# Kernel optimization log

Measured on AMD Instinct MI355X. Metric: run time of the kernel, lower is better.

## Reference

```python
import jax, jax.numpy as jnp
import numpy as np

AH, AW = 7, 7          # aligned_height, aligned_width
SCALE = 0.0625         # spatial_scale = 1/16
B, C, H, W, K = 2, 512, 64, 64, 2000


def setup_inputs() -> dict:
    key = jax.random.key(0)
    k1, k2, k3, k4 = jax.random.split(key, 4)
    features = jax.random.normal(k1, (B, C, H, W), dtype=jnp.float32)
    img = H / SCALE  # image-space extent = 1024
    bidx = jax.random.randint(k2, (K,), 0, B).astype(jnp.float32)
    xy1 = jax.random.uniform(k3, (K, 2), minval=0.0, maxval=img * 0.7)
    wh = jax.random.uniform(k4, (K, 2), minval=img * 0.05, maxval=img * 0.3)
    xy2 = jnp.minimum(xy1 + wh, img - 1.0)
    rois = jnp.concatenate(
        [bidx[:, None], xy1[:, 0:1], xy1[:, 1:2], xy2[:, 0:1], xy2[:, 1:2]], axis=1
    )
    return {"features": features, "rois": rois}


def _roi_align(features, rois, ph, pw, scale):
    # one bilinear sample per output pixel on a ph x pw grid, with
    # bin_size = roi_size / (p - 1), zero for out-of-bounds sample points.
    _, _, Hf, Wf = features.shape
    b = rois[:, 0].astype(jnp.int32)
    x1 = rois[:, 1] * scale
    y1 = rois[:, 2] * scale
    x2 = rois[:, 3] * scale
    y2 = rois[:, 4] * scale
    roi_w = jnp.maximum(x2 - x1, 0.0)
    roi_h = jnp.maximum(y2 - y1, 0.0)
    bin_h = roi_h / (ph - 1.0)
    bin_w = roi_w / (pw - 1.0)
    h = y1[:, None] + jnp.arange(ph, dtype=jnp.float32) * bin_h[:, None]  # [K,ph]
    w = x1[:, None] + jnp.arange(pw, dtype=jnp.float32) * bin_w[:, None]  # [K,pw]
    hs = jnp.minimum(jnp.floor(h), Hf - 2.0)
    ws = jnp.minimum(jnp.floor(w), Wf - 2.0)
    hr = h - hs  # interpolation ratios (match CUDA kernel exactly)
    wr = w - ws
    hi = jnp.clip(hs, 0, Hf - 2).astype(jnp.int32)
    wi = jnp.clip(ws, 0, Wf - 2).astype(jnp.int32)
    bK = b[:, None, None]          # [K,1,1]
    hK = hi[:, :, None]            # [K,ph,1]
    wK = wi[:, None, :]            # [K,1,pw]
    # advanced indexing: corner gathers -> [K,ph,pw,C]
    v00 = features[bK, :, hK, wK]
    v01 = features[bK, :, hK, wK + 1]
    v10 = features[bK, :, hK + 1, wK]
    v11 = features[bK, :, hK + 1, wK + 1]
    hrE = hr[:, :, None, None]
    wrE = wr[:, None, :, None]
    val = (v00 * (1 - hrE) * (1 - wrE)
           + v01 * (1 - hrE) * wrE
           + v10 * hrE * (1 - wrE)
           + v11 * hrE * wrE)
    valid = ((h >= 0) & (h < Hf))[:, :, None] & ((w >= 0) & (w < Wf))[:, None, :]
    val = jnp.where(valid[..., None], val, 0.0)
    return jnp.transpose(val, (0, 3, 1, 2))  # [K,C,ph,pw]


def reference(features, rois):
    # sample on (AH+1)x(AW+1) grid, then avg_pool2d(kernel=2, stride=1)
    x = _roi_align(features, rois, AH + 1, AW + 1, SCALE)  # [K,C,8,8]
    out = (x[:, :, :-1, :-1] + x[:, :, :-1, 1:]
           + x[:, :, 1:, :-1] + x[:, :, 1:, 1:]) * 0.25    # [K,C,7,7]
    return out
```

## Files before the change

kernel.cpp:

```cpp
#include <hip/hip_runtime.h>

#define HF 64
#define WF 64
#define CCH 512

typedef float f32x4 __attribute__((ext_vector_type(4)));

__device__ __forceinline__ unsigned short f32_to_bf16(float f) {
    unsigned int x = __float_as_uint(f);
    unsigned int r = (x + 0x7FFFu + ((x >> 16) & 1u)) >> 16;
    return (unsigned short)r;
}
__device__ __forceinline__ float bf16_to_f32(unsigned short u) {
    return __uint_as_float(((unsigned int)u) << 16);
}

__global__ __launch_bounds__(256) void nchw_to_nhwc_bf16(const float* __restrict__ src,
                                                         unsigned short* __restrict__ dst) {
    __shared__ float tile[32][33];
    const int hw0 = blockIdx.x * 32;
    const int c0  = blockIdx.y * 32;
    const int b   = blockIdx.z;
    const int tx  = threadIdx.x & 31;
    const int ty  = threadIdx.x >> 5;
    const float*    s = src + (size_t)b * CCH * (HF * WF);
    unsigned short* d = dst + (size_t)b * (HF * WF) * CCH;
#pragma unroll
    for (int i = 0; i < 32; i += 8)
        tile[ty + i][tx] = s[(size_t)(c0 + ty + i) * (HF * WF) + hw0 + tx];
    __syncthreads();
#pragma unroll
    for (int i = 0; i < 32; i += 8)
        d[(size_t)(hw0 + ty + i) * CCH + c0 + tx] = f32_to_bf16(tile[tx][ty + i]);
}

__global__ __launch_bounds__(256) void roialign_bf16(const unsigned short* __restrict__ ft,
                                                     const float* __restrict__ rois,
                                                     float* __restrict__ out) {
    __shared__ __align__(16) float sbuf[256 * 49];

    const int blk   = blockIdx.x;
    const int k     = blk >> 1;
    const int chunk = blk & 1;
    const int tid   = threadIdx.x;
    const int c     = chunk * 256 + tid;

    const float* r = rois + (size_t)k * 5;
    const int   b  = (int)r[0];
    const float x1 = r[1] * 0.0625f;
    const float y1 = r[2] * 0.0625f;
    const float x2 = r[3] * 0.0625f;
    const float y2 = r[4] * 0.0625f;
    const float bin_h = fmaxf(y2 - y1, 0.0f) / 7.0f;
    const float bin_w = fmaxf(x2 - x1, 0.0f) / 7.0f;

    int   hi_[8]; float hr_[8]; float fvh[8];
    int   wi_[8]; float wr_[8]; float fvw[8];
    unsigned colc[8];
#pragma unroll
    for (int i = 0; i < 8; ++i) {
        float h  = y1 + (float)i * bin_h;
        float hs = fminf(floorf(h), 62.0f);
        hr_[i]   = h - hs;
        hi_[i]   = (int)fminf(fmaxf(hs, 0.0f), 62.0f);
        fvh[i]   = (h >= 0.0f && h < 64.0f) ? 1.0f : 0.0f;
        float w  = x1 + (float)i * bin_w;
        float ws = fminf(floorf(w), 62.0f);
        wr_[i]   = w - ws;
        wi_[i]   = (int)fminf(fmaxf(ws, 0.0f), 62.0f);
        fvw[i]   = (w >= 0.0f && w < 64.0f) ? 1.0f : 0.0f;
        colc[i]  = (unsigned)(wi_[i] * CCH + c);
    }
    const unsigned bBase = (unsigned)(b * HF * WF * CCH);

    float TL[8], TR[8], BL[8], BR[8];
    int curR = -1000;

    float  prev[8];
    float* srow = sbuf + tid * 49;

#pragma unroll
    for (int i = 0; i < 8; ++i) {
        const int rr = hi_[i];
        if (rr == curR) {
        } else if (rr == curR + 1) {
#pragma unroll
            for (int j = 0; j < 8; ++j) { TL[j] = BL[j]; TR[j] = BR[j]; }
            const unsigned rb = bBase + (unsigned)((rr + 1) * WF * CCH);
#pragma unroll
            for (int j = 0; j < 8; ++j) {
                BL[j] = bf16_to_f32(ft[rb + colc[j]]);
                BR[j] = bf16_to_f32(ft[rb + colc[j] + CCH]);
            }
        } else {
            const unsigned rt = bBase + (unsigned)(rr * WF * CCH);
            const unsigned rb = rt + (unsigned)(WF * CCH);
#pragma unroll
            for (int j = 0; j < 8; ++j) {
                TL[j] = bf16_to_f32(ft[rt + colc[j]]);
                TR[j] = bf16_to_f32(ft[rt + colc[j] + CCH]);
            }
#pragma unroll
            for (int j = 0; j < 8; ++j) {
                BL[j] = bf16_to_f32(ft[rb + colc[j]]);
                BR[j] = bf16_to_f32(ft[rb + colc[j] + CCH]);
            }
        }
        curR = rr;

        float cur[8];
#pragma unroll
        for (int j = 0; j < 8; ++j) {
            const float top = TL[j] + wr_[j] * (TR[j] - TL[j]);
            const float bot = BL[j] + wr_[j] * (BR[j] - BL[j]);
            const float v   = top + hr_[i] * (bot - top);
            cur[j] = v * (fvh[i] * fvw[j]);
        }
        if (i > 0) {
#pragma unroll
            for (int j = 0; j < 7; ++j)
                srow[(i - 1) * 7 + j] =
                    0.25f * (prev[j] + prev[j + 1] + cur[j] + cur[j + 1]);
        }
#pragma unroll
        for (int j = 0; j < 8; ++j) prev[j] = cur[j];
    }

    __builtin_amdgcn_wave_barrier();

    const int wid  = tid >> 6;
    const int lane = tid & 63;
    float* obase = out + ((size_t)k * CCH + (size_t)chunk * 256 + (size_t)wid * 64) * 49;
    const f32x4* s4 = reinterpret_cast<const f32x4*>(sbuf + (size_t)wid * 64 * 49);
    f32x4*       o4 = reinterpret_cast<f32x4*>(obase);
    for (int idx = lane; idx < 784; idx += 64)
        __builtin_nontemporal_store(s4[idx], &o4[idx]);
}

__global__ __launch_bounds__(256) void roialign_f32_nchw(const float* __restrict__ ft,
                                                         const float* __restrict__ rois,
                                                         float* __restrict__ out) {
    __shared__ __align__(16) float sbuf[256 * 49];
    const int blk   = blockIdx.x;
    const int k     = blk >> 1;
    const int chunk = blk & 1;
    const int tid   = threadIdx.x;
    const int c     = chunk * 256 + tid;

    const float* r = rois + (size_t)k * 5;
    const int   b  = (int)r[0];
    const float x1 = r[1] * 0.0625f;
    const float y1 = r[2] * 0.0625f;
    const float x2 = r[3] * 0.0625f;
    const float y2 = r[4] * 0.0625f;
    const float bin_h = fmaxf(y2 - y1, 0.0f) / 7.0f;
    const float bin_w = fmaxf(x2 - x1, 0.0f) / 7.0f;

    int hi_[8]; float hr_[8]; float fvh[8];
    int wi_[8]; float wr_[8]; float fvw[8];
#pragma unroll
    for (int i = 0; i < 8; ++i) {
        float h  = y1 + (float)i * bin_h;
        float hs = fminf(floorf(h), 62.0f);
        hr_[i] = h - hs;
        hi_[i] = (int)fminf(fmaxf(hs, 0.0f), 62.0f);
        fvh[i] = (h >= 0.0f && h < 64.0f) ? 1.0f : 0.0f;
        float w  = x1 + (float)i * bin_w;
        float ws = fminf(floorf(w), 62.0f);
        wr_[i] = w - ws;
        wi_[i] = (int)fminf(fmaxf(ws, 0.0f), 62.0f);
        fvw[i] = (w >= 0.0f && w < 64.0f) ? 1.0f : 0.0f;
    }

    float prev[8];
    float* srow = sbuf + tid * 49;
#pragma unroll
    for (int i = 0; i < 8; ++i) {
        float cur[8];
#pragma unroll
        for (int j = 0; j < 8; ++j) {
            size_t o00 = (size_t)(b * CCH + c) * (HF * WF) + hi_[i] * WF + wi_[j];
            const float v00 = ft[o00];
            const float v01 = ft[o00 + 1];
            const float v10 = ft[o00 + WF];
            const float v11 = ft[o00 + WF + 1];
            const float top = v00 + wr_[j] * (v01 - v00);
            const float bot = v10 + wr_[j] * (v11 - v10);
            const float v   = top + hr_[i] * (bot - top);
            cur[j] = v * (fvh[i] * fvw[j]);
        }
        if (i > 0) {
#pragma unroll
            for (int j = 0; j < 7; ++j)
                srow[(i - 1) * 7 + j] =
                    0.25f * (prev[j] + prev[j + 1] + cur[j] + cur[j + 1]);
        }
#pragma unroll
        for (int j = 0; j < 8; ++j) prev[j] = cur[j];
    }
    __syncthreads();
    float* obase = out + ((size_t)k * CCH + (size_t)chunk * 256) * 49;
    const f32x4* s4 = reinterpret_cast<const f32x4*>(sbuf);
    f32x4*       o4 = reinterpret_cast<f32x4*>(obase);
    for (int idx = tid; idx < 3136; idx += 256) o4[idx] = s4[idx];
}

extern "C" void kernel_launch(void* const* d_in, const int* in_sizes, int n_in,
                              void* d_out, int out_size, void* d_ws, size_t ws_size,
                              hipStream_t stream) {
    const float* feat = (const float*)d_in[0];
    const float* rois = (const float*)d_in[1];
    float*       out  = (float*)d_out;

    const int B = in_sizes[0] / (CCH * HF * WF);
    const int K = in_sizes[1] / 5;

    const size_t tbytes = (size_t)B * CCH * HF * WF * sizeof(unsigned short);
    if (ws_size >= tbytes) {
        unsigned short* ftr = (unsigned short*)d_ws;
        dim3 tg((HF * WF) / 32, CCH / 32, B);
        nchw_to_nhwc_bf16<<<tg, 256, 0, stream>>>(feat, ftr);
        roialign_bf16<<<K * 2, 256, 0, stream>>>(ftr, rois, out);
    } else {
        roialign_f32_nchw<<<K * 2, 256, 0, stream>>>(feat, rois, out);
    }
}
```

Before: 66.43 us.

## Prefetch next ROI row corners and scalarize uniform row indices

The bf16 ROI-align kernel now loads the next bottom-row corners one iteration ahead, so the gathers overlap with the current row's interpolation. Row indices, ratios and column offsets are forced into scalar registers with readfirstlane, and launch bounds request 3 waves per SIMD. This targets gather latency and VGPR pressure, at the cost of extra registers for the prefetch buffers and possible spilling under the tighter launch bound.

New measurement: 71.49 us. +7.6%, slower.

```diff
diff --git a/kernel.cpp b/kernel.cpp
--- a/kernel.cpp
+++ b/kernel.cpp
@@ -13,6 +13,10 @@
 }
 __device__ __forceinline__ float bf16_to_f32(unsigned short u) {
     return __uint_as_float(((unsigned int)u) << 16);
+}
+__device__ __forceinline__ int   rfl_i(int x)   { return __builtin_amdgcn_readfirstlane(x); }
+__device__ __forceinline__ float rfl_f(float x) {
+    return __int_as_float(__builtin_amdgcn_readfirstlane(__float_as_int(x)));
 }
 
 __global__ __launch_bounds__(256) void nchw_to_nhwc_bf16(const float* __restrict__ src,
@@ -34,9 +38,9 @@
         d[(size_t)(hw0 + ty + i) * CCH + c0 + tx] = f32_to_bf16(tile[tx][ty + i]);
 }
 
-__global__ __launch_bounds__(256) void roialign_bf16(const unsigned short* __restrict__ ft,
-                                                     const float* __restrict__ rois,
-                                                     float* __restrict__ out) {
+__global__ __launch_bounds__(256, 3) void roialign_bf16(const unsigned short* __restrict__ ft,
+                                                        const float* __restrict__ rois,
+                                                        float* __restrict__ out) {
     __shared__ __align__(16) float sbuf[256 * 49];
 
     const int blk   = blockIdx.x;
@@ -54,67 +58,86 @@
     const float bin_h = fmaxf(y2 - y1, 0.0f) / 7.0f;
     const float bin_w = fmaxf(x2 - x1, 0.0f) / 7.0f;
 
-    int   hi_[8]; float hr_[8]; float fvh[8];
-    int   wi_[8]; float wr_[8]; float fvw[8];
-    unsigned colc[8];
+    int   hiS[8];
+    float hrS[8], fvhS[8];
+    int   colS[8];
+    float wrV[8], fvwV[8];
 #pragma unroll
     for (int i = 0; i < 8; ++i) {
         float h  = y1 + (float)i * bin_h;
         float hs = fminf(floorf(h), 62.0f);
-        hr_[i]   = h - hs;
-        hi_[i]   = (int)fminf(fmaxf(hs, 0.0f), 62.0f);
-        fvh[i]   = (h >= 0.0f && h < 64.0f) ? 1.0f : 0.0f;
+        float hr = h - hs;
+        int   hi = (int)fminf(fmaxf(hs, 0.0f), 62.0f);
+        float fh = (h >= 0.0f && h < 64.0f) ? 1.0f : 0.0f;
         float w  = x1 + (float)i * bin_w;
         float ws = fminf(floorf(w), 62.0f);
-        wr_[i]   = w - ws;
-        wi_[i]   = (int)fminf(fmaxf(ws, 0.0f), 62.0f);
-        fvw[i]   = (w >= 0.0f && w < 64.0f) ? 1.0f : 0.0f;
-        colc[i]  = (unsigned)(wi_[i] * CCH + c);
-    }
-    const unsigned bBase = (unsigned)(b * HF * WF * CCH);
+        wrV[i]   = w - ws;
+        int   wi = (int)fminf(fmaxf(ws, 0.0f), 62.0f);
+        fvwV[i]  = (w >= 0.0f && w < 64.0f) ? 1.0f : 0.0f;
+        hiS[i]   = rfl_i(hi);
+        hrS[i]   = rfl_f(hr);
+        fvhS[i]  = rfl_f(fh);
+        colS[i]  = rfl_i(wi) * CCH;
+    }
+    const int rowBase = rfl_i(b) * HF * WF * CCH;
 
     float TL[8], TR[8], BL[8], BR[8];
-    int curR = -1000;
+    float nBL[8], nBR[8];
+
+    {
+        const int rT = rowBase + hiS[0] * (WF * CCH);
+        const int rB = rT + WF * CCH;
+#pragma unroll
+        for (int j = 0; j < 8; ++j) {
+            TL[j] = bf16_to_f32(ft[(unsigned)(rT + colS[j] + c)]);
+            TR[j] = bf16_to_f32(ft[(unsigned)(rT + colS[j] + CCH + c)]);
+            BL[j] = bf16_to_f32(ft[(unsigned)(rB + colS[j] + c)]);
+            BR[j] = bf16_to_f32(ft[(unsigned)(rB + colS[j] + CCH + c)]);
+        }
+    }
 
     float  prev[8];
     float* srow = sbuf + tid * 49;
 
 #pragma unroll
     for (int i = 0; i < 8; ++i) {
-        const int rr = hi_[i];
-        if (rr == curR) {
-        } else if (rr == curR + 1) {
-#pragma unroll
-            for (int j = 0; j < 8; ++j) { TL[j] = BL[j]; TR[j] = BR[j]; }
-            const unsigned rb = bBase + (unsigned)((rr + 1) * WF * CCH);
-#pragma unroll
-            for (int j = 0; j < 8; ++j) {
-                BL[j] = bf16_to_f32(ft[rb + colc[j]]);
-                BR[j] = bf16_to_f32(ft[rb + colc[j] + CCH]);
+        if (i > 0) {
+            if (hiS[i] == hiS[i - 1]) {
+            } else if (hiS[i] == hiS[i - 1] + 1) {
+#pragma unroll
+                for (int j = 0; j < 8; ++j) {
+                    TL[j] = BL[j]; TR[j] = BR[j];
+                    BL[j] = nBL[j]; BR[j] = nBR[j];
+                }
+            } else {
+                const int rT = rowBase + hiS[i] * (WF * CCH);
+#pragma unroll
+                for (int j = 0; j < 8; ++j) {
+                    TL[j] = bf16_to_f32(ft[(unsigned)(rT + colS[j] + c)]);
+                    TR[j] = bf16_to_f32(ft[(unsigned)(rT + colS[j] + CCH + c)]);
+                    BL[j] = nBL[j]; BR[j] = nBR[j];
+                }
             }
-        } else {
-            const unsigned rt = bBase + (unsigned)(rr * WF * CCH);
-            const unsigned rb = rt + (unsigned)(WF * CCH);
-#pragma unroll
-            for (int j = 0; j < 8; ++j) {
-                TL[j] = bf16_to_f32(ft[rt + colc[j]]);
-                TR[j] = bf16_to_f32(ft[rt + colc[j] + CCH]);
+        }
+
+        if (i < 7) {
+            if (hiS[i + 1] != hiS[i]) {
+                const int rB = rowBase + (hiS[i + 1] + 1) * (WF * CCH);
+#pragma unroll
+                for (int j = 0; j < 8; ++j) {
+                    nBL[j] = bf16_to_f32(ft[(unsigned)(rB + colS[j] + c)]);
+                    nBR[j] = bf16_to_f32(ft[(unsigned)(rB + colS[j] + CCH + c)]);
+                }
             }
-#pragma unroll
-            for (int j = 0; j < 8; ++j) {
-                BL[j] = bf16_to_f32(ft[rb + colc[j]]);
-                BR[j] = bf16_to_f32(ft[rb + colc[j] + CCH]);
-            }
-        }
-        curR = rr;
+        }
 
         float cur[8];
 #pragma unroll
         for (int j = 0; j < 8; ++j) {
-            const float top = TL[j] + wr_[j] * (TR[j] - TL[j]);
-            const float bot = BL[j] + wr_[j] * (BR[j] - BL[j]);
-            const float v   = top + hr_[i] * (bot - top);
-            cur[j] = v * (fvh[i] * fvw[j]);
+            const float top = TL[j] + wrV[j] * (TR[j] - TL[j]);
+            const float bot = BL[j] + wrV[j] * (BR[j] - BL[j]);
+            const float v   = top + hrS[i] * (bot - top);
+            cur[j] = (v * fvwV[j]) * fvhS[i];
         }
         if (i > 0) {
 #pragma unroll
```

## Replace per-ROI grid with persistent wave-level work-stealing kernel

Applied to the files above, without the earlier changes.

The bf16 ROI-align kernel becomes persistent: 768 blocks of 4 waves each pull (roi, 64-channel slice) items from a global atomic counter, and each wave computes and stores its slice independently. This removes per-block launch and tail costs and balances load across CUs. It adds a memset launch, one atomic per work item, and a launch_bounds occupancy hint of 3 blocks, all of which could offset the gains.

After: 244.6 us. +268.2%, slower.

```diff
diff --git a/kernel.cpp b/kernel.cpp
--- a/kernel.cpp
+++ b/kernel.cpp
@@ -34,107 +34,117 @@
         d[(size_t)(hw0 + ty + i) * CCH + c0 + tx] = f32_to_bf16(tile[tx][ty + i]);
 }
 
-__global__ __launch_bounds__(256) void roialign_bf16(const unsigned short* __restrict__ ft,
-                                                     const float* __restrict__ rois,
-                                                     float* __restrict__ out) {
+__global__ __launch_bounds__(256, 3) void roialign_persist(const unsigned short* __restrict__ ft,
+                                                           const float* __restrict__ rois,
+                                                           float* __restrict__ out,
+                                                           int* __restrict__ counter,
+                                                           int nItems) {
     __shared__ __align__(16) float sbuf[256 * 49];
-
-    const int blk   = blockIdx.x;
-    const int k     = blk >> 1;
-    const int chunk = blk & 1;
-    const int tid   = threadIdx.x;
-    const int c     = chunk * 256 + tid;
-
-    const float* r = rois + (size_t)k * 5;
-    const int   b  = (int)r[0];
-    const float x1 = r[1] * 0.0625f;
-    const float y1 = r[2] * 0.0625f;
-    const float x2 = r[3] * 0.0625f;
-    const float y2 = r[4] * 0.0625f;
-    const float bin_h = fmaxf(y2 - y1, 0.0f) / 7.0f;
-    const float bin_w = fmaxf(x2 - x1, 0.0f) / 7.0f;
-
-    int   hi_[8]; float hr_[8]; float fvh[8];
-    int   wi_[8]; float wr_[8]; float fvw[8];
-    unsigned colc[8];
-#pragma unroll
-    for (int i = 0; i < 8; ++i) {
-        float h  = y1 + (float)i * bin_h;
-        float hs = fminf(floorf(h), 62.0f);
-        hr_[i]   = h - hs;
-        hi_[i]   = (int)fminf(fmaxf(hs, 0.0f), 62.0f);
-        fvh[i]   = (h >= 0.0f && h < 64.0f) ? 1.0f : 0.0f;
-        float w  = x1 + (float)i * bin_w;
-        float ws = fminf(floorf(w), 62.0f);
-        wr_[i]   = w - ws;
-        wi_[i]   = (int)fminf(fmaxf(ws, 0.0f), 62.0f);
-        fvw[i]   = (w >= 0.0f && w < 64.0f) ? 1.0f : 0.0f;
-        colc[i]  = (unsigned)(wi_[i] * CCH + c);
-    }
-    const unsigned bBase = (unsigned)(b * HF * WF * CCH);
-
-    float TL[8], TR[8], BL[8], BR[8];
-    int curR = -1000;
-
-    float  prev[8];
-    float* srow = sbuf + tid * 49;
-
-#pragma unroll
-    for (int i = 0; i < 8; ++i) {
-        const int rr = hi_[i];
-        if (rr == curR) {
-        } else if (rr == curR + 1) {
-#pragma unroll
-            for (int j = 0; j < 8; ++j) { TL[j] = BL[j]; TR[j] = BR[j]; }
-            const unsigned rb = bBase + (unsigned)((rr + 1) * WF * CCH);
+    const int lane = threadIdx.x & 63;
+    const int wid  = threadIdx.x >> 6;
+    float* wbuf = sbuf + (size_t)wid * 64 * 49;
+
+    for (;;) {
+        int item = 0;
+        if (lane == 0) item = atomicAdd(counter, 1);
+        item = __builtin_amdgcn_readfirstlane(item);
+        if (item >= nItems) break;
+
+        const int k   = item >> 3;
+        const int sub = item & 7;
+        const int c   = sub * 64 + lane;
+
+        const float* r = rois + (size_t)k * 5;
+        const int   b  = (int)r[0];
+        const float x1 = r[1] * 0.0625f;
+        const float y1 = r[2] * 0.0625f;
+        const float x2 = r[3] * 0.0625f;
+        const float y2 = r[4] * 0.0625f;
+        const float bin_h = fmaxf(y2 - y1, 0.0f) / 7.0f;
+        const float bin_w = fmaxf(x2 - x1, 0.0f) / 7.0f;
+
+        int   hi_[8]; float hr_[8]; float fvh[8];
+        float wr_[8]; float fvw[8];
+        unsigned colc[8];
+#pragma unroll
+        for (int i = 0; i < 8; ++i) {
+            float h  = y1 + (float)i * bin_h;
+            float hs = fminf(floorf(h), 62.0f);
+            hr_[i]   = h - hs;
+            hi_[i]   = (int)fminf(fmaxf(hs, 0.0f), 62.0f);
+            fvh[i]   = (h >= 0.0f && h < 64.0f) ? 1.0f : 0.0f;
+            float w  = x1 + (float)i * bin_w;
+            float ws = fminf(floorf(w), 62.0f);
+            wr_[i]   = w - ws;
+            int   wi = (int)fminf(fmaxf(ws, 0.0f), 62.0f);
+            fvw[i]   = (w >= 0.0f && w < 64.0f) ? 1.0f : 0.0f;
+            colc[i]  = (unsigned)(wi * CCH + c);
+        }
+        const unsigned bBase = (unsigned)(b * HF * WF * CCH);
+
+        float TL[8], TR[8], BL[8], BR[8];
+        int curR = -1000;
+
+        float  prev[8];
+        float* srow = wbuf + lane * 49;
+
+#pragma unroll
+        for (int i = 0; i < 8; ++i) {
+            const int rr = hi_[i];
+            if (rr == curR) {
+            } else if (rr == curR + 1) {
+#pragma unroll
+                for (int j = 0; j < 8; ++j) { TL[j] = BL[j]; TR[j] = BR[j]; }
+                const unsigned rb = bBase + (unsigned)((rr + 1) * WF * CCH);
+#pragma unroll
+                for (int j = 0; j < 8; ++j) {
+                    BL[j] = bf16_to_f32(ft[rb + colc[j]]);
+                    BR[j] = bf16_to_f32(ft[rb + colc[j] + CCH]);
+                }
+            } else {
+                const unsigned rt = bBase + (unsigned)(rr * WF * CCH);
+                const unsigned rb = rt + (unsigned)(WF * CCH);
+#pragma unroll
+                for (int j = 0; j < 8; ++j) {
+                    TL[j] = bf16_to_f32(ft[rt + colc[j]]);
+                    TR[j] = bf16_to_f32(ft[rt + colc[j] + CCH]);
+                }
+#pragma unroll
+                for (int j = 0; j < 8; ++j) {
+                    BL[j] = bf16_to_f32(ft[rb + colc[j]]);
+                    BR[j] = bf16_to_f32(ft[rb + colc[j] + CCH]);
+                }
+            }
+            curR = rr;
+
+            float cur[8];
 #pragma unroll
             for (int j = 0; j < 8; ++j) {
-                BL[j] = bf16_to_f32(ft[rb + colc[j]]);
-                BR[j] = bf16_to_f32(ft[rb + colc[j] + CCH]);
+                const float top = TL[j] + wr_[j] * (TR[j] - TL[j]);
+                const float bot = BL[j] + wr_[j] * (BR[j] - BL[j]);
+                const float v   = top + hr_[i] * (bot - top);
+                cur[j] = v * (fvh[i] * fvw[j]);
             }
-        } else {
-            const unsigned rt = bBase + (unsigned)(rr * WF * CCH);
-            const unsigned rb = rt + (unsigned)(WF * CCH);
-#pragma unroll
-            for (int j = 0; j < 8; ++j) {
-                TL[j] = bf16_to_f32(ft[rt + colc[j]]);
-                TR[j] = bf16_to_f32(ft[rt + colc[j] + CCH]);
+            if (i > 0) {
+#pragma unroll
+                for (int j = 0; j < 7; ++j)
+                    srow[(i - 1) * 7 + j] =
+                        0.25f * (prev[j] + prev[j + 1] + cur[j] + cur[j + 1]);
             }
 #pragma unroll
-            for (int j = 0; j < 8; ++j) {
-                BL[j] = bf16_to_f32(ft[rb + colc[j]]);
-                BR[j] = bf16_to_f32(ft[rb + colc[j] + CCH]);
-            }
-        }
-        curR = rr;
-
-        float cur[8];
-#pragma unroll
-        for (int j = 0; j < 8; ++j) {
-            const float top = TL[j] + wr_[j] * (TR[j] - TL[j]);
-            const float bot = BL[j] + wr_[j] * (BR[j] - BL[j]);
-            const float v   = top + hr_[i] * (bot - top);
-            cur[j] = v * (fvh[i] * fvw[j]);
-        }
-        if (i > 0) {
-#pragma unroll
-            for (int j = 0; j < 7; ++j)
-                srow[(i - 1) * 7 + j] =
-                    0.25f * (prev[j] + prev[j + 1] + cur[j] + cur[j + 1]);
-        }
-#pragma unroll
-        for (int j = 0; j < 8; ++j) prev[j] = cur[j];
-    }
-
-    __builtin_amdgcn_wave_barrier();
-
-    const int wid  = tid >> 6;
-    const int lane = tid & 63;
-    float* obase = out + ((size_t)k * CCH + (size_t)chunk * 256 + (size_t)wid * 64) * 49;
-    const f32x4* s4 = reinterpret_cast<const f32x4*>(sbuf + (size_t)wid * 64 * 49);
-    f32x4*       o4 = reinterpret_cast<f32x4*>(obase);
-    for (int idx = lane; idx < 784; idx += 64)
-        __builtin_nontemporal_store(s4[idx], &o4[idx]);
+            for (int j = 0; j < 8; ++j) prev[j] = cur[j];
+        }
+
+        __builtin_amdgcn_wave_barrier();
+
+        float* obase = out + ((size_t)k * CCH + (size_t)sub * 64) * 49;
+        const f32x4* s4 = reinterpret_cast<const f32x4*>(wbuf);
+        f32x4*       o4 = reinterpret_cast<f32x4*>(obase);
+        for (int idx = lane; idx < 784; idx += 64)
+            __builtin_nontemporal_store(s4[idx], &o4[idx]);
+
+        __builtin_amdgcn_wave_barrier();
+    }
 }
 
 __global__ __launch_bounds__(256) void roialign_f32_nchw(const float* __restrict__ ft,
@@ -215,12 +225,17 @@
     const int B = in_sizes[0] / (CCH * HF * WF);
     const int K = in_sizes[1] / 5;
 
-    const size_t tbytes = (size_t)B * CCH * HF * WF * sizeof(unsigned short);
-    if (ws_size >= tbytes) {
+    const size_t featBytes = (size_t)B * CCH * HF * WF * sizeof(unsigned short);
+    const size_t ctrOff    = (featBytes + 127) & ~(size_t)127;
+
+    if (ws_size >= ctrOff + 128) {
         unsigned short* ftr = (unsigned short*)d_ws;
+        int*            ctr = (int*)((char*)d_ws + ctrOff);
+        hipMemsetAsync(ctr, 0, sizeof(int), stream);
         dim3 tg((HF * WF) / 32, CCH / 32, B);
         nchw_to_nhwc_bf16<<<tg, 256, 0, stream>>>(feat, ftr);
-        roialign_bf16<<<K * 2, 256, 0, stream>>>(ftr, rois, out);
+        const int nItems = K * (CCH / 64);
+        roialign_persist<<<768, 256, 0, stream>>>(ftr, rois, out, ctr, nItems);
     } else {
         roialign_f32_nchw<<<K * 2, 256, 0, stream>>>(feat, rois, out);
     }
```

## Split ROI rows across two waves and pre-interpolate columns to cut registers

Applied to the files above, without the earlier changes.

Replaces the 256-thread roialign kernel with a 128-thread block per (roi, 64-channel slice). Wave 0 computes output rows 0-2 and wave 1 computes rows 3-6, with one sample row recomputed at the boundary. Horizontal interpolation now happens right after loading, so only two row arrays are kept instead of four corner arrays, and the launch bounds ask for higher occupancy. This adds more parallel work and memory-level parallelism per ROI, at the cost of some duplicated loads and index math plus a block-wide sync.

After: 209.8 us. +215.9%, slower.

```diff
diff --git a/kernel.cpp b/kernel.cpp
--- a/kernel.cpp
+++ b/kernel.cpp
@@ -34,16 +34,91 @@
         d[(size_t)(hw0 + ty + i) * CCH + c0 + tx] = f32_to_bf16(tile[tx][ty + i]);
 }
 
-__global__ __launch_bounds__(256) void roialign_bf16(const unsigned short* __restrict__ ft,
-                                                     const float* __restrict__ rois,
-                                                     float* __restrict__ out) {
-    __shared__ __align__(16) float sbuf[256 * 49];
-
-    const int blk   = blockIdx.x;
-    const int k     = blk >> 1;
-    const int chunk = blk & 1;
-    const int tid   = threadIdx.x;
-    const int c     = chunk * 256 + tid;
+template <int I0, int I1>
+__device__ __forceinline__ void roi_part(const unsigned short* __restrict__ ft,
+                                         float* __restrict__ srow,
+                                         float x1, float y1, float bin_h, float bin_w,
+                                         unsigned bBase, int c) {
+    float wr_[8], fvw[8]; unsigned colc[8];
+#pragma unroll
+    for (int j = 0; j < 8; ++j) {
+        float w  = x1 + (float)j * bin_w;
+        float ws = fminf(floorf(w), 62.0f);
+        wr_[j]   = w - ws;
+        int   wi = (int)fminf(fmaxf(ws, 0.0f), 62.0f);
+        fvw[j]   = (w >= 0.0f && w < 64.0f) ? 1.0f : 0.0f;
+        colc[j]  = (unsigned)(wi * CCH + c);
+    }
+
+    float rowT[8], rowB[8];
+    int   curR = -1000;
+    float prev[8];
+
+#pragma unroll
+    for (int i = I0; i < I1; ++i) {
+        float h  = y1 + (float)i * bin_h;
+        float hs = fminf(floorf(h), 62.0f);
+        float hr = h - hs;
+        int   rr = (int)fminf(fmaxf(hs, 0.0f), 62.0f);
+        float fh = (h >= 0.0f && h < 64.0f) ? 1.0f : 0.0f;
+
+        if (rr == curR) {
+        } else if (rr == curR + 1) {
+#pragma unroll
+            for (int j = 0; j < 8; ++j) rowT[j] = rowB[j];
+            const unsigned rb = bBase + (unsigned)((rr + 1) * WF * CCH);
+#pragma unroll
+            for (int j = 0; j < 8; ++j) {
+                const float L = bf16_to_f32(ft[rb + colc[j]]);
+                const float R = bf16_to_f32(ft[rb + colc[j] + CCH]);
+                rowB[j] = L + wr_[j] * (R - L);
+            }
+        } else {
+            const unsigned rt = bBase + (unsigned)(rr * WF * CCH);
+            const unsigned rb = rt + (unsigned)(WF * CCH);
+#pragma unroll
+            for (int j = 0; j < 8; ++j) {
+                const float L = bf16_to_f32(ft[rt + colc[j]]);
+                const float R = bf16_to_f32(ft[rt + colc[j] + CCH]);
+                rowT[j] = L + wr_[j] * (R - L);
+            }
+#pragma unroll
+            for (int j = 0; j < 8; ++j) {
+                const float L = bf16_to_f32(ft[rb + colc[j]]);
+                const float R = bf16_to_f32(ft[rb + colc[j] + CCH]);
+                rowB[j] = L + wr_[j] * (R - L);
+            }
+        }
+        curR = rr;
+
+        float cur[8];
+#pragma unroll
+        for (int j = 0; j < 8; ++j) {
+            const float v = rowT[j] + hr * (rowB[j] - rowT[j]);
+            cur[j] = v * (fh * fvw[j]);
+        }
+        if (i > I0) {
+#pragma unroll
+            for (int j = 0; j < 7; ++j)
+                srow[(i - 1) * 7 + j] =
+                    0.25f * (prev[j] + prev[j + 1] + cur[j] + cur[j + 1]);
+        }
+#pragma unroll
+        for (int j = 0; j < 8; ++j) prev[j] = cur[j];
+    }
+}
+
+__global__ __launch_bounds__(128, 6) void roialign_split(const unsigned short* __restrict__ ft,
+                                                         const float* __restrict__ rois,
+                                                         float* __restrict__ out) {
+    __shared__ __align__(16) float sbuf[64 * 49];
+    const int tid  = threadIdx.x;
+    const int lane = tid & 63;
+    const int wid  = tid >> 6;
+    const int blk  = blockIdx.x;
+    const int k    = blk >> 3;
+    const int sub  = blk & 7;
+    const int c    = sub * 64 + lane;
 
     const float* r = rois + (size_t)k * 5;
     const int   b  = (int)r[0];
@@ -53,87 +128,19 @@
     const float y2 = r[4] * 0.0625f;
     const float bin_h = fmaxf(y2 - y1, 0.0f) / 7.0f;
     const float bin_w = fmaxf(x2 - x1, 0.0f) / 7.0f;
-
-    int   hi_[8]; float hr_[8]; float fvh[8];
-    int   wi_[8]; float wr_[8]; float fvw[8];
-    unsigned colc[8];
-#pragma unroll
-    for (int i = 0; i < 8; ++i) {
-        float h  = y1 + (float)i * bin_h;
-        float hs = fminf(floorf(h), 62.0f);
-        hr_[i]   = h - hs;
-        hi_[i]   = (int)fminf(fmaxf(hs, 0.0f), 62.0f);
-        fvh[i]   = (h >= 0.0f && h < 64.0f) ? 1.0f : 0.0f;
-        float w  = x1 + (float)i * bin_w;
-        float ws = fminf(floorf(w), 62.0f);
-        wr_[i]   = w - ws;
-        wi_[i]   = (int)fminf(fmaxf(ws, 0.0f), 62.0f);
-        fvw[i]   = (w >= 0.0f && w < 64.0f) ? 1.0f : 0.0f;
-        colc[i]  = (unsigned)(wi_[i] * CCH + c);
-    }
     const unsigned bBase = (unsigned)(b * HF * WF * CCH);
 
-    float TL[8], TR[8], BL[8], BR[8];
-    int curR = -1000;
-
-    float  prev[8];
-    float* srow = sbuf + tid * 49;
-
-#pragma unroll
-    for (int i = 0; i < 8; ++i) {
-        const int rr = hi_[i];
-        if (rr == curR) {
-        } else if (rr == curR + 1) {
-#pragma unroll
-            for (int j = 0; j < 8; ++j) { TL[j] = BL[j]; TR[j] = BR[j]; }
-            const unsigned rb = bBase + (unsigned)((rr + 1) * WF * CCH);
-#pragma unroll
-            for (int j = 0; j < 8; ++j) {
-                BL[j] = bf16_to_f32(ft[rb + colc[j]]);
-                BR[j] = bf16_to_f32(ft[rb + colc[j] + CCH]);
-            }
-        } else {
-            const unsigned rt = bBase + (unsigned)(rr * WF * CCH);
-            const unsigned rb = rt + (unsigned)(WF * CCH);
-#pragma unroll
-            for (int j = 0; j < 8; ++j) {
-                TL[j] = bf16_to_f32(ft[rt + colc[j]]);
-                TR[j] = bf16_to_f32(ft[rt + colc[j] + CCH]);
-            }
-#pragma unroll
-            for (int j = 0; j < 8; ++j) {
-                BL[j] = bf16_to_f32(ft[rb + colc[j]]);
-                BR[j] = bf16_to_f32(ft[rb + colc[j] + CCH]);
-            }
-        }
-        curR = rr;
-
-        float cur[8];
-#pragma unroll
-        for (int j = 0; j < 8; ++j) {
-            const float top = TL[j] + wr_[j] * (TR[j] - TL[j]);
-            const float bot = BL[j] + wr_[j] * (BR[j] - BL[j]);
-            const float v   = top + hr_[i] * (bot - top);
-            cur[j] = v * (fvh[i] * fvw[j]);
-        }
-        if (i > 0) {
-#pragma unroll
-            for (int j = 0; j < 7; ++j)
-                srow[(i - 1) * 7 + j] =
-                    0.25f * (prev[j] + prev[j + 1] + cur[j] + cur[j + 1]);
-        }
-#pragma unroll
-        for (int j = 0; j < 8; ++j) prev[j] = cur[j];
-    }
-
-    __builtin_amdgcn_wave_barrier();
-
-    const int wid  = tid >> 6;
-    const int lane = tid & 63;
-    float* obase = out + ((size_t)k * CCH + (size_t)chunk * 256 + (size_t)wid * 64) * 49;
-    const f32x4* s4 = reinterpret_cast<const f32x4*>(sbuf + (size_t)wid * 64 * 49);
+    float* srow = sbuf + lane * 49;
+
+    if (wid == 0) roi_part<0, 4>(ft, srow, x1, y1, bin_h, bin_w, bBase, c);
+    else          roi_part<3, 8>(ft, srow, x1, y1, bin_h, bin_w, bBase, c);
+
+    __syncthreads();
+
+    float* obase = out + ((size_t)k * CCH + (size_t)sub * 64) * 49;
+    const f32x4* s4 = reinterpret_cast<const f32x4*>(sbuf);
     f32x4*       o4 = reinterpret_cast<f32x4*>(obase);
-    for (int idx = lane; idx < 784; idx += 64)
+    for (int idx = tid; idx < 784; idx += 128)
         __builtin_nontemporal_store(s4[idx], &o4[idx]);
 }
 
@@ -215,12 +222,12 @@
     const int B = in_sizes[0] / (CCH * HF * WF);
     const int K = in_sizes[1] / 5;
 
-    const size_t tbytes = (size_t)B * CCH * HF * WF * sizeof(unsigned short);
-    if (ws_size >= tbytes) {
+    const size_t featBytes = (size_t)B * CCH * HF * WF * sizeof(unsigned short);
+    if (ws_size >= featBytes) {
         unsigned short* ftr = (unsigned short*)d_ws;
         dim3 tg((HF * WF) / 32, CCH / 32, B);
         nchw_to_nhwc_bf16<<<tg, 256, 0, stream>>>(feat, ftr);
-        roialign_bf16<<<K * 2, 256, 0, stream>>>(ftr, rois, out);
+        roialign_split<<<K * 8, 128, 0, stream>>>(ftr, rois, out);
     } else {
         roialign_f32_nchw<<<K * 2, 256, 0, stream>>>(feat, rois, out);
     }
```
